# Kernel tuning notes

Measured on AMD Instinct MI355X. Metric: run time of the kernel, lower is better.

The kernel has to match this reference:

```python
import jax, jax.numpy as jnp
import numpy as np

B, D, T, H = 1024, 128, 256, 64  # batch, input_dim, seq_len, hidden_dim


def _lstm_layer(x_proj, w_hh):
    """x_proj: [B, T, 4H] precomputed input projection (incl. both biases).
    Returns (all hidden states [B, T, H], final hidden [B, H])."""
    b = x_proj.shape[0]
    h0 = jnp.zeros((b, H), x_proj.dtype)
    c0 = jnp.zeros((b, H), x_proj.dtype)

    def step(carry, xt):
        h, c = carry
        gates = xt + h @ w_hh.T  # [B, 4H]; PyTorch gate order i, f, g, o
        i, f, g, o = jnp.split(gates, 4, axis=-1)
        i = jax.nn.sigmoid(i)
        f = jax.nn.sigmoid(f)
        g = jnp.tanh(g)
        o = jax.nn.sigmoid(o)
        c = f * c + i * g
        h = o * jnp.tanh(c)
        return (h, c), h

    (hT, _), ys = jax.lax.scan(step, (h0, c0), x_proj.transpose(1, 0, 2))
    return ys.transpose(1, 0, 2), hT


def setup_inputs() -> dict:
    key = jax.random.key(0)
    ks = jax.random.split(key, 11)
    s = 1.0 / np.sqrt(H)  # PyTorch LSTM init scale
    return {
        "x": jax.random.normal(ks[0], (B, D, T), jnp.float32),
        "w_ih0": jax.random.normal(ks[1], (4 * H, D), jnp.float32) * s,
        "w_hh0": jax.random.normal(ks[2], (4 * H, H), jnp.float32) * s,
        "b_ih0": jax.random.normal(ks[3], (4 * H,), jnp.float32) * s,
        "b_hh0": jax.random.normal(ks[4], (4 * H,), jnp.float32) * s,
        "w_ih1": jax.random.normal(ks[5], (4 * H, H), jnp.float32) * s,
        "w_hh1": jax.random.normal(ks[6], (4 * H, H), jnp.float32) * s,
        "b_ih1": jax.random.normal(ks[7], (4 * H,), jnp.float32) * s,
        "b_hh1": jax.random.normal(ks[8], (4 * H,), jnp.float32) * s,
        "w_fc": jax.random.normal(ks[9], (D, H), jnp.float32) * s,
        "b_fc": jax.random.normal(ks[10], (D,), jnp.float32) * s,
    }


def reference(x, w_ih0, w_hh0, b_ih0, b_hh0, w_ih1, w_hh1, b_ih1, b_hh1, w_fc, b_fc):
    # x: [B, input_dim, T] -> permute(0, 2, 1) -> [B, T, input_dim]
    xt = x.transpose(0, 2, 1)
    # Layer 0: precompute input projection for all timesteps (one big GEMM)
    xp0 = xt @ w_ih0.T + (b_ih0 + b_hh0)  # [B, T, 4H]
    ys0, _ = _lstm_layer(xp0, w_hh0)
    # Inter-layer dropout(p=0.3) is identity in eval/inference mode.
    xp1 = ys0 @ w_ih1.T + (b_ih1 + b_hh1)  # [B, T, 4H]
    _, hT = _lstm_layer(xp1, w_hh1)
    # Final-timestep linear head: lstm_out[:, -1, :] == final hidden state hT
    scores = hT @ w_fc.T + b_fc  # [B, input_dim]
    return scores
```

## Files before the change

### kernel.cpp

```cpp
#include <hip/hip_runtime.h>

#define T_SEQ 256
#define PH  72
#define HSZ 1152
#define XRW 144
#define XSL 584

typedef float f32x4 __attribute__((ext_vector_type(4)));
typedef _Float16 f16x8 __attribute__((ext_vector_type(8)));

__device__ __forceinline__ float sigmoid_f(float x) {
    float e = __builtin_amdgcn_exp2f(-1.4426950408889634f * x);
    return __builtin_amdgcn_rcpf(1.0f + e);
}
__device__ __forceinline__ float tanh_f(float x) {
    float e = __builtin_amdgcn_exp2f(-2.8853900817779268f * x);
    return 2.0f * __builtin_amdgcn_rcpf(1.0f + e) - 1.0f;
}
__device__ __forceinline__ f16x8 load_frag16h(const float* wp, int n, int K, int k0) {
    const float* wf = wp + (size_t)n * K + k0;
    f16x8 h;
    #pragma unroll
    for (int j = 0; j < 8; ++j) h[j] = (_Float16)wf[j];
    return h;
}
__device__ __forceinline__ void load_frag16(const float* wp, int n, int K, int k0,
                                            f16x8& hi, f16x8& lo) {
    const float* wf = wp + (size_t)n * K + k0;
    #pragma unroll
    for (int j = 0; j < 8; ++j) {
        const float v = wf[j];
        const _Float16 h = (_Float16)v;
        hi[j] = h;
        lo[j] = (_Float16)(v - (float)h);
    }
}
__device__ __forceinline__ void gload16(const void* g, void* l) {
    __builtin_amdgcn_global_load_lds(
        (const __attribute__((address_space(1))) unsigned int*)g,
        (__attribute__((address_space(3))) unsigned int*)l, 16, 0, 0);
}

#define MFMA16(a, b, c) __builtin_amdgcn_mfma_f32_16x16x32_f16(a, b, c, 0, 0, 0)

__global__ __launch_bounds__(512, 2) void rec_fused(
    const float* __restrict__ x,
    const float* __restrict__ wih0, const float* __restrict__ whh0,
    const float* __restrict__ bih0, const float* __restrict__ bhh0,
    const float* __restrict__ wih1, const float* __restrict__ whh1,
    const float* __restrict__ bih1, const float* __restrict__ bhh1,
    const float* __restrict__ wfc,  const float* __restrict__ bfc,
    float* __restrict__ out)
{
    __shared__ float    xs32[4 * 2048];
    __shared__ _Float16 xh[32 * XSL];
    __shared__ _Float16 h0[2 * HSZ], h1[2 * HSZ];
    const int tid = threadIdx.x, lane = tid & 63, w = tid >> 6;
    const int l16 = lane & 15, quad = lane >> 4, k0 = quad * 8;
    const int wl = w & 3;
    const bool is1 = (w < 4);
    const int bb  = blockIdx.x & 63;
    const int sub = blockIdx.x >> 6;

    const float* xrow = x + (size_t)(bb * 16 + wl * 4 + sub) * 128 * 256;

    f16x8 fA[4][2], fAl[4][2], fB[4][4];
    float gb[4];
    #pragma unroll
    for (int g = 0; g < 4; ++g) {
        const int n = g * 64 + wl * 16 + l16;
        if (is1) {
            #pragma unroll
            for (int ks = 0; ks < 2; ++ks) {
                fA[g][ks] = load_frag16h(wih1, n, 64, ks * 32 + k0);
                load_frag16(whh1, n, 64, ks * 32 + k0, fB[g][ks], fB[g][2 + ks]);
            }
            gb[g] = bih1[n] + bhh1[n];
        } else {
            #pragma unroll
            for (int ks = 0; ks < 4; ++ks)
                fB[g][ks] = load_frag16h(wih0, n, 128, ks * 32 + k0);
            #pragma unroll
            for (int ks = 0; ks < 2; ++ks)
                load_frag16(whh0, n, 64, ks * 32 + k0, fA[g][ks], fAl[g][ks]);
            gb[g] = bih0[n] + bhh0[n];
        }
    }
    for (int i = tid; i < 2 * HSZ; i += 512) { h0[i] = (_Float16)0.f; h1[i] = (_Float16)0.f; }
    float c = 0.f;
    f32x4 xacc[4];

    auto convert_rows = [&](int cc, int ib0, int nib) {
        const int sb = (cc & 1) * 16;
        const int tq = lane & 3;
        for (int ib = ib0; ib < ib0 + nib; ++ib) {
            const float4 v = *(const float4*)&xs32[wl * 2048 + ib * 256 + lane * 4];
            const int d = ib * 16 + (lane >> 2);
            const float vv[4] = {v.x, v.y, v.z, v.w};
            #pragma unroll
            for (int j = 0; j < 4; ++j)
                xh[(sb + tq * 4 + j) * XSL + wl * XRW + d] = (_Float16)vv[j];
        }
    };
    auto issue_chunk = [&](int cc) {
        #pragma unroll
        for (int ib = 0; ib < 8; ++ib)
            gload16(xrow + (size_t)(ib * 16 + (lane >> 2)) * 256 + cc * 16 + (lane & 3) * 4,
                    (char*)xs32 + wl * 8192 + ib * 1024);
    };
    auto precompute_x = [&](int slot) {
        f16x8 ax[4];
        #pragma unroll
        for (int ks = 0; ks < 4; ++ks)
            ax[ks] = *(const f16x8*)&xh[slot * XSL + (l16 >> 2) * XRW + ks * 32 + k0];
        #pragma unroll
        for (int g = 0; g < 4; ++g) xacc[g] = (f32x4){gb[g], 0.f, 0.f, 0.f};
        #pragma unroll
        for (int g = 0; g < 4; ++g)
            #pragma unroll
            for (int ks = 0; ks < 4; ++ks)
                xacc[g] = MFMA16(ax[ks], fB[g][ks], xacc[g]);
    };

    if (!is1) issue_chunk(0);
    __syncthreads();
    if (!is1) { convert_rows(0, 0, 8); issue_chunk(1); }
    __syncthreads();

    if (!is1) {
        precompute_x(0);
        const float gi = sigmoid_f(xacc[0][0]);
        const float gg = tanh_f(xacc[2][0]);
        const float go = sigmoid_f(xacc[3][0]);
        c = gi * gg;
        h0[(quad * 4) * PH + wl * 16 + l16] = (_Float16)(go * tanh_f(c));
        precompute_x(1);
    }
    __syncthreads();

    for (int t = 0; t < 255; ++t) {
        const int s0 = t & 1, s1 = s0 ^ 1;
        const int tn = t + 1;
        if (is1) {
            f16x8 ah[2], bh[2];
            #pragma unroll
            for (int ks = 0; ks < 2; ++ks) {
                ah[ks] = *(const f16x8*)&h0[s0 * HSZ + l16 * PH + ks * 32 + k0];
                bh[ks] = *(const f16x8*)&h1[s1 * HSZ + l16 * PH + ks * 32 + k0];
            }
            f32x4 accA[4], accB[4];
            #pragma unroll
            for (int g = 0; g < 4; ++g) {
                accA[g] = (f32x4){gb[g], 0.f, 0.f, 0.f};
                accB[g] = (f32x4){0.f, 0.f, 0.f, 0.f};
            }
            #pragma unroll
            for (int g = 0; g < 4; ++g)
                #pragma unroll
                for (int ks = 0; ks < 2; ++ks) {
                    accA[g] = MFMA16(ah[ks], fA[g][ks], accA[g]);
                    accA[g] = MFMA16(bh[ks], fB[g][ks], accA[g]);
                    accB[g] = MFMA16(bh[ks], fB[g][2 + ks], accB[g]);
                }
            const float gi = sigmoid_f(accA[0][0] + accB[0][0]);
            const float gf = sigmoid_f(accA[1][0] + accB[1][0]);
            const float gg = tanh_f(accA[2][0] + accB[2][0]);
            const float go = sigmoid_f(accA[3][0] + accB[3][0]);
            c = gf * c + gi * gg;
            h1[s0 * HSZ + (quad * 4) * PH + wl * 16 + l16] =
                (_Float16)(go * tanh_f(c));
        } else {
            if ((tn & 15) == 0 && tn < 240)
                issue_chunk((tn >> 4) + 1);
            f16x8 ah[2];
            #pragma unroll
            for (int ks = 0; ks < 2; ++ks)
                ah[ks] = *(const f16x8*)&h0[s0 * HSZ + l16 * PH + ks * 32 + k0];
            f32x4 acc[4];
            #pragma unroll
            for (int g = 0; g < 4; ++g) acc[g] = xacc[g];
            #pragma unroll
            for (int g = 0; g < 4; ++g)
                #pragma unroll
                for (int ks = 0; ks < 2; ++ks) {
                    acc[g] = MFMA16(ah[ks], fA[g][ks], acc[g]);
                    acc[g] = MFMA16(ah[ks], fAl[g][ks], acc[g]);
                }
            const float gi = sigmoid_f(acc[0][0]);
            const float gf = sigmoid_f(acc[1][0]);
            const float gg = tanh_f(acc[2][0]);
            const float go = sigmoid_f(acc[3][0]);
            c = gf * c + gi * gg;
            h0[s1 * HSZ + (quad * 4) * PH + wl * 16 + l16] =
                (_Float16)(go * tanh_f(c));
            const int m16 = tn & 15;
            if (m16 >= 8 && m16 < 12 && tn < 248)
                convert_rows((tn >> 4) + 1, (m16 - 8) * 2, 2);
            if (tn < 255) {
                const int tn2 = tn + 1;
                precompute_x(((tn2 >> 4) & 1) * 16 + (tn2 & 15));
            }
        }
        __syncthreads();
    }

    if (is1) {
        f16x8 ah[2], bh[2];
        #pragma unroll
        for (int ks = 0; ks < 2; ++ks) {
            ah[ks] = *(const f16x8*)&h0[HSZ + l16 * PH + ks * 32 + k0];
            bh[ks] = *(const f16x8*)&h1[l16 * PH + ks * 32 + k0];
        }
        f32x4 accA[4], accB[4];
        #pragma unroll
        for (int g = 0; g < 4; ++g) {
            accA[g] = (f32x4){gb[g], 0.f, 0.f, 0.f};
            accB[g] = (f32x4){0.f, 0.f, 0.f, 0.f};
        }
        #pragma unroll
        for (int g = 0; g < 4; ++g)
            #pragma unroll
            for (int ks = 0; ks < 2; ++ks) {
                accA[g] = MFMA16(ah[ks], fA[g][ks], accA[g]);
                accA[g] = MFMA16(bh[ks], fB[g][ks], accA[g]);
                accB[g] = MFMA16(bh[ks], fB[g][2 + ks], accB[g]);
            }
        const float gi = sigmoid_f(accA[0][0] + accB[0][0]);
        const float gf = sigmoid_f(accA[1][0] + accB[1][0]);
        const float gg = tanh_f(accA[2][0] + accB[2][0]);
        const float go = sigmoid_f(accA[3][0] + accB[3][0]);
        c = gf * c + gi * gg;
        h1[HSZ + (quad * 4) * PH + wl * 16 + l16] = (_Float16)(go * tanh_f(c));
    }
    __syncthreads();

    const int n   = tid & 127;
    const int sel = tid >> 7;
    float s = 0.f;
    for (int k = 0; k < 64; ++k)
        s += (float)h1[HSZ + (sel * 4) * PH + k] * wfc[n * 64 + k];
    out[(size_t)(bb * 16 + sel * 4 + sub) * 128 + n] = s + bfc[n];
}

extern "C" void kernel_launch(void* const* d_in, const int* in_sizes, int n_in,
                              void* d_out, int out_size, void* d_ws, size_t ws_size,
                              hipStream_t stream) {
    const float* x     = (const float*)d_in[0];
    const float* wih0  = (const float*)d_in[1];
    const float* whh0  = (const float*)d_in[2];
    const float* bih0  = (const float*)d_in[3];
    const float* bhh0  = (const float*)d_in[4];
    const float* wih1  = (const float*)d_in[5];
    const float* whh1  = (const float*)d_in[6];
    const float* bih1  = (const float*)d_in[7];
    const float* bhh1  = (const float*)d_in[8];
    const float* wfc   = (const float*)d_in[9];
    const float* bfc   = (const float*)d_in[10];
    float* out = (float*)d_out;

    rec_fused<<<256, 512, 0, stream>>>(x, wih0, whh0, bih0, bhh0,
                                       wih1, whh1, bih1, bhh1, wfc, bfc, out);
}
```

Before: 381.4 us.

## Split layer-0 input projection into dedicated waves with LDS ring buffer

After: 365.8 us. 4.1% less time.

```diff
diff --git a/kernel.cpp b/kernel.cpp
--- a/kernel.cpp
+++ b/kernel.cpp
@@ -1,6 +1,5 @@
 #include <hip/hip_runtime.h>
 
-#define T_SEQ 256
 #define PH  72
 #define HSZ 1152
 #define XRW 144
@@ -43,7 +42,7 @@
 
 #define MFMA16(a, b, c) __builtin_amdgcn_mfma_f32_16x16x32_f16(a, b, c, 0, 0, 0)
 
-__global__ __launch_bounds__(512, 2) void rec_fused(
+__global__ __launch_bounds__(768, 3) void rec_fused(
     const float* __restrict__ x,
     const float* __restrict__ wih0, const float* __restrict__ whh0,
     const float* __restrict__ bih0, const float* __restrict__ bhh0,
@@ -54,18 +53,20 @@
 {
     __shared__ float    xs32[4 * 2048];
     __shared__ _Float16 xh[32 * XSL];
+    __shared__ float    xpl[4 * 1024];
     __shared__ _Float16 h0[2 * HSZ], h1[2 * HSZ];
     const int tid = threadIdx.x, lane = tid & 63, w = tid >> 6;
     const int l16 = lane & 15, quad = lane >> 4, k0 = quad * 8;
     const int wl = w & 3;
-    const bool is1 = (w < 4);
+    const int role = w >> 2;
+    const bool is1 = (role == 0), is0 = (role == 1), isP = (role == 2);
     const int bb  = blockIdx.x & 63;
     const int sub = blockIdx.x >> 6;
 
     const float* xrow = x + (size_t)(bb * 16 + wl * 4 + sub) * 128 * 256;
 
-    f16x8 fA[4][2], fAl[4][2], fB[4][4];
-    float gb[4];
+    f16x8 fA[4][2], fB[4][4];
+    float gb[4] = {0.f, 0.f, 0.f, 0.f};
     #pragma unroll
     for (int g = 0; g < 4; ++g) {
         const int n = g * 64 + wl * 16 + l16;
@@ -76,19 +77,19 @@
                 load_frag16(whh1, n, 64, ks * 32 + k0, fB[g][ks], fB[g][2 + ks]);
             }
             gb[g] = bih1[n] + bhh1[n];
+        } else if (is0) {
+            #pragma unroll
+            for (int ks = 0; ks < 2; ++ks)
+                load_frag16(whh0, n, 64, ks * 32 + k0, fA[g][ks], fB[g][2 + ks]);
         } else {
             #pragma unroll
             for (int ks = 0; ks < 4; ++ks)
                 fB[g][ks] = load_frag16h(wih0, n, 128, ks * 32 + k0);
-            #pragma unroll
-            for (int ks = 0; ks < 2; ++ks)
-                load_frag16(whh0, n, 64, ks * 32 + k0, fA[g][ks], fAl[g][ks]);
             gb[g] = bih0[n] + bhh0[n];
         }
     }
-    for (int i = tid; i < 2 * HSZ; i += 512) { h0[i] = (_Float16)0.f; h1[i] = (_Float16)0.f; }
+    for (int i = tid; i < 2 * HSZ; i += 768) { h0[i] = (_Float16)0.f; h1[i] = (_Float16)0.f; }
     float c = 0.f;
-    f32x4 xacc[4];
 
     auto convert_rows = [&](int cc, int ib0, int nib) {
         const int sb = (cc & 1) * 16;
@@ -108,33 +109,38 @@
             gload16(xrow + (size_t)(ib * 16 + (lane >> 2)) * 256 + cc * 16 + (lane & 3) * 4,
                     (char*)xs32 + wl * 8192 + ib * 1024);
     };
-    auto precompute_x = [&](int slot) {
+    auto compute_xp = [&](int tp) {
+        const int fs = ((tp >> 4) & 1) * 16 + (tp & 15);
         f16x8 ax[4];
         #pragma unroll
         for (int ks = 0; ks < 4; ++ks)
-            ax[ks] = *(const f16x8*)&xh[slot * XSL + (l16 >> 2) * XRW + ks * 32 + k0];
-        #pragma unroll
-        for (int g = 0; g < 4; ++g) xacc[g] = (f32x4){gb[g], 0.f, 0.f, 0.f};
+            ax[ks] = *(const f16x8*)&xh[fs * XSL + (l16 >> 2) * XRW + ks * 32 + k0];
+        f32x4 pa[4];
+        #pragma unroll
+        for (int g = 0; g < 4; ++g) pa[g] = (f32x4){gb[g], 0.f, 0.f, 0.f};
         #pragma unroll
         for (int g = 0; g < 4; ++g)
             #pragma unroll
             for (int ks = 0; ks < 4; ++ks)
-                xacc[g] = MFMA16(ax[ks], fB[g][ks], xacc[g]);
+                pa[g] = MFMA16(ax[ks], fB[g][ks], pa[g]);
+        f32x4 o;
+        o[0] = pa[0][0]; o[1] = pa[1][0]; o[2] = pa[2][0]; o[3] = pa[3][0];
+        *(f32x4*)&xpl[(((tp & 3) * 4 + wl) * 64 + lane) * 4] = o;
     };
 
-    if (!is1) issue_chunk(0);
-    __syncthreads();
-    if (!is1) { convert_rows(0, 0, 8); issue_chunk(1); }
-    __syncthreads();
-
-    if (!is1) {
-        precompute_x(0);
-        const float gi = sigmoid_f(xacc[0][0]);
-        const float gg = tanh_f(xacc[2][0]);
-        const float go = sigmoid_f(xacc[3][0]);
+    if (isP) issue_chunk(0);
+    __syncthreads();
+    if (isP) { convert_rows(0, 0, 8); issue_chunk(1); }
+    __syncthreads();
+    if (isP) { compute_xp(0); compute_xp(1); }
+    __syncthreads();
+    if (is0) {
+        const f32x4 xp4 = *(const f32x4*)&xpl[(wl * 64 + lane) * 4];
+        const float gi = sigmoid_f(xp4[0]);
+        const float gg = tanh_f(xp4[2]);
+        const float go = sigmoid_f(xp4[3]);
         c = gi * gg;
         h0[(quad * 4) * PH + wl * 16 + l16] = (_Float16)(go * tanh_f(c));
-        precompute_x(1);
     }
     __syncthreads();
 
@@ -169,37 +175,41 @@
             c = gf * c + gi * gg;
             h1[s0 * HSZ + (quad * 4) * PH + wl * 16 + l16] =
                 (_Float16)(go * tanh_f(c));
+        } else if (is0) {
+            const f32x4 xp4 =
+                *(const f32x4*)&xpl[(((tn & 3) * 4 + wl) * 64 + lane) * 4];
+            f16x8 ah[2];
+            #pragma unroll
+            for (int ks = 0; ks < 2; ++ks)
+                ah[ks] = *(const f16x8*)&h0[s0 * HSZ + l16 * PH + ks * 32 + k0];
+            f32x4 accA[4], accB[4];
+            #pragma unroll
+            for (int g = 0; g < 4; ++g) {
+                accA[g] = (f32x4){xp4[g], 0.f, 0.f, 0.f};
+                accB[g] = (f32x4){0.f, 0.f, 0.f, 0.f};
+            }
+            #pragma unroll
+            for (int g = 0; g < 4; ++g)
+                #pragma unroll
+                for (int ks = 0; ks < 2; ++ks) {
+                    accA[g] = MFMA16(ah[ks], fA[g][ks], accA[g]);
+                    accB[g] = MFMA16(ah[ks], fB[g][2 + ks], accB[g]);
+                }
+            const float gi = sigmoid_f(accA[0][0] + accB[0][0]);
+            const float gf = sigmoid_f(accA[1][0] + accB[1][0]);
+            const float gg = tanh_f(accA[2][0] + accB[2][0]);
+            const float go = sigmoid_f(accA[3][0] + accB[3][0]);
+            c = gf * c + gi * gg;
+            h0[s1 * HSZ + (quad * 4) * PH + wl * 16 + l16] =
+                (_Float16)(go * tanh_f(c));
         } else {
             if ((tn & 15) == 0 && tn < 240)
                 issue_chunk((tn >> 4) + 1);
-            f16x8 ah[2];
-            #pragma unroll
-            for (int ks = 0; ks < 2; ++ks)
-                ah[ks] = *(const f16x8*)&h0[s0 * HSZ + l16 * PH + ks * 32 + k0];
-            f32x4 acc[4];
-            #pragma unroll
-            for (int g = 0; g < 4; ++g) acc[g] = xacc[g];
-            #pragma unroll
-            for (int g = 0; g < 4; ++g)
-                #pragma unroll
-                for (int ks = 0; ks < 2; ++ks) {
-                    acc[g] = MFMA16(ah[ks], fA[g][ks], acc[g]);
-                    acc[g] = MFMA16(ah[ks], fAl[g][ks], acc[g]);
-                }
-            const float gi = sigmoid_f(acc[0][0]);
-            const float gf = sigmoid_f(acc[1][0]);
-            const float gg = tanh_f(acc[2][0]);
-            const float go = sigmoid_f(acc[3][0]);
-            c = gf * c + gi * gg;
-            h0[s1 * HSZ + (quad * 4) * PH + wl * 16 + l16] =
-                (_Float16)(go * tanh_f(c));
             const int m16 = tn & 15;
             if (m16 >= 8 && m16 < 12 && tn < 248)
                 convert_rows((tn >> 4) + 1, (m16 - 8) * 2, 2);
-            if (tn < 255) {
-                const int tn2 = tn + 1;
-                precompute_x(((tn2 >> 4) & 1) * 16 + (tn2 & 15));
-            }
+            const int tp = t + 2;
+            if (tp <= 255) compute_xp(tp);
         }
         __syncthreads();
     }
@@ -234,12 +244,14 @@
     }
     __syncthreads();
 
-    const int n   = tid & 127;
-    const int sel = tid >> 7;
-    float s = 0.f;
-    for (int k = 0; k < 64; ++k)
-        s += (float)h1[HSZ + (sel * 4) * PH + k] * wfc[n * 64 + k];
-    out[(size_t)(bb * 16 + sel * 4 + sub) * 128 + n] = s + bfc[n];
+    if (tid < 512) {
+        const int n   = tid & 127;
+        const int sel = tid >> 7;
+        float s = 0.f;
+        for (int k = 0; k < 64; ++k)
+            s += (float)h1[HSZ + (sel * 4) * PH + k] * wfc[n * 64 + k];
+        out[(size_t)(bb * 16 + sel * 4 + sub) * 128 + n] = s + bfc[n];
+    }
 }
 
 extern "C" void kernel_launch(void* const* d_in, const int* in_sizes, int n_in,
@@ -258,6 +270,6 @@
     const float* bfc   = (const float*)d_in[10];
     float* out = (float*)d_out;
 
-    rec_fused<<<256, 512, 0, stream>>>(x, wih0, whh0, bih0, bhh0,
+    rec_fused<<<256, 768, 0, stream>>>(x, wih0, whh0, bih0, bhh0,
                                        wih1, whh1, bih1, bhh1, wfc, bfc, out);
 }
```
